# Performance work log

Hardware: AMD Instinct MI355X
Metric: run time of the kernel (lower is better)

The kernel has to match this reference:

```python
import jax, jax.numpy as jnp
import numpy as np

B, L, D, H, HD, K, MLP = 4, 2048, 1024, 16, 64, 24, 4096


def setup_inputs() -> dict:
    key = jax.random.key(0)
    ks = jax.random.split(key, 17)
    f32 = jnp.float32
    rn = lambda k, s, sc=1.0: jax.random.normal(k, s, dtype=f32) * sc
    return {
        'inputs': rn(ks[0], (B, L, D)),
        'eig_vals': jax.random.uniform(ks[1], (K,), dtype=f32),  # positive eigenvalues
        'eig_vecs': rn(ks[2], (L, K), 1.0 / np.sqrt(L)),
        'w_filters': rn(ks[3], (K, D), 1.0 / np.sqrt(K)),        # lecun_normal-ish
        'w_inputs': rn(ks[4], (D, D), 1.0 / np.sqrt(D)),
        'ln1_scale': jnp.ones((D,), f32),
        'ln1_bias': jnp.zeros((D,), f32),
        'wq': rn(ks[5], (D, H, HD), 1.0 / np.sqrt(D)),
        'wk': rn(ks[6], (D, H, HD), 1.0 / np.sqrt(D)),
        'wv': rn(ks[7], (D, H, HD), 1.0 / np.sqrt(D)),
        'wo': rn(ks[8], (H, HD, D), 1.0 / np.sqrt(D)),
        'ln2_scale': jnp.ones((D,), f32),
        'ln2_bias': jnp.zeros((D,), f32),
        'mlp_w1': rn(ks[9], (D, MLP), 1.0 / np.sqrt(D)),
        'mlp_b1': jnp.zeros((MLP,), f32),
        'mlp_w2': rn(ks[10], (MLP, D), 1.0 / np.sqrt(MLP)),
        'mlp_b2': jnp.zeros((D,), f32),
    }


def _layer_norm(x, scale, bias, eps=1e-6):
    m = jnp.mean(x, axis=-1, keepdims=True)
    v = jnp.var(x, axis=-1, keepdims=True)
    return (x - m) * jax.lax.rsqrt(v + eps) * scale + bias


def reference(inputs, eig_vals, eig_vecs, w_filters, w_inputs,
              ln1_scale, ln1_bias, wq, wk, wv, wo,
              ln2_scale, ln2_bias, mlp_w1, mlp_b1, mlp_w2, mlp_b2):
    seq = inputs.shape[1]
    # --- STU spectral long convolution ---
    rescaled = eig_vecs * eig_vals[None, :] ** 0.25            # [L,K]
    filters = jnp.einsum('lk,kd->ld', rescaled, w_filters)      # [L,D]
    xi = jnp.einsum('bli,id->bld', inputs, w_inputs)            # [B,L,D]
    # causal per-channel conv: out[b,l,d] = sum_t filters[t,d]*xi[b,l-t,d]
    # == full convolve truncated to first L; do it as one batched FFT conv.
    n = 2 * seq
    F = jnp.fft.rfft(filters, n=n, axis=0)                      # [n//2+1, D]
    X = jnp.fft.rfft(xi, n=n, axis=1)                           # [B, n//2+1, D]
    projection = jnp.fft.irfft(X * F[None], n=n, axis=1)[:, :seq, :]
    stu_outs = projection                                       # make_stu_residual=False

    # --- self attention (pre-LN) ---
    x = _layer_norm(stu_outs, ln1_scale, ln1_bias)
    hd = wq.shape[-1]
    q = jnp.einsum('bld,dhk->blhk', x, wq) / jnp.sqrt(jnp.asarray(hd, x.dtype))
    k = jnp.einsum('bld,dhk->blhk', x, wk)
    v = jnp.einsum('bld,dhk->blhk', x, wv)
    attn = jax.nn.softmax(jnp.einsum('bqhk,bshk->bhqs', q, k), axis=-1)
    a = jnp.einsum('bhqs,bshk->bqhk', attn, v)
    a = jnp.einsum('bqhk,hkd->bqd', a, wo)
    x = a + stu_outs

    # --- MLP block (pre-LN) ---
    y = _layer_norm(x, ln2_scale, ln2_bias)
    y = jax.nn.gelu(jnp.einsum('bld,df->blf', y, mlp_w1) + mlp_b1)
    y = jnp.einsum('blf,fd->bld', y, mlp_w2) + mlp_b2
    return x + y
```

## Files before the change

kernel.cpp:

```cpp
#include <hip/hip_runtime.h>
#include <math.h>

#define B_ 4
#define L_ 2048
#define D_ 1024
#define H_ 16
#define HD_ 64
#define K_ 24
#define MLP_ 4096

typedef unsigned short u16;
typedef short s16x8 __attribute__((ext_vector_type(8)));
typedef float fx4 __attribute__((ext_vector_type(4)));
typedef _Float16 h2 __attribute__((ext_vector_type(2)));

__device__ __forceinline__ u16 f2bf(float f) {
    unsigned u = __float_as_uint(f);
    unsigned r = (u + 0x7fff + ((u >> 16) & 1)) >> 16;
    return (u16)r;
}

__device__ __forceinline__ u16 f2h(float f) {
    _Float16 hv = (_Float16)f;
    return __builtin_bit_cast(u16, hv);
}

__device__ __forceinline__ float gelu_t(float x) {
    float u = 0.7978845608028654f * (x + 0.044715f * x * x * x);
    return x / (1.f + __expf(-2.f * u));
}

__device__ __forceinline__ void gload_lds16(const void* g, void* l) {
    __builtin_amdgcn_global_load_lds(
        (const __attribute__((address_space(1))) unsigned int*)g,
        (__attribute__((address_space(3))) unsigned int*)l, 16, 0, 0);
}

#define SBAR() do { __builtin_amdgcn_sched_barrier(0); \
                    __builtin_amdgcn_s_barrier(); \
                    __builtin_amdgcn_sched_barrier(0); } while (0)

__global__ __launch_bounds__(256) void filters_T(const float* __restrict__ eig_vals,
                                                 const float* __restrict__ eig_vecs,
                                                 const float* __restrict__ w_filters,
                                                 u16* __restrict__ outT) {
    int l0 = blockIdx.x * 64, d0 = blockIdx.y * 64;
    __shared__ float ev25[K_];
    __shared__ float rr[64][25];
    __shared__ float wfs[K_][64];
    int tid = threadIdx.x;
    if (tid < K_) ev25[tid] = powf(eig_vals[tid], 0.25f);
    __syncthreads();
    for (int i = tid; i < 64 * K_; i += 256)
        rr[i / K_][i % K_] = eig_vecs[l0 * K_ + i];
    for (int i = tid; i < K_ * 64; i += 256) {
        int k = i >> 6, dd = i & 63;
        wfs[k][dd] = ev25[k] * w_filters[k * D_ + d0 + dd];
    }
    __syncthreads();
    int lane = tid & 63, w = tid >> 6;
    float acc[16];
#pragma unroll
    for (int i = 0; i < 16; i++) acc[i] = 0.f;
#pragma unroll
    for (int k = 0; k < K_; k++) {
        float rv = rr[lane][k];
#pragma unroll
        for (int i = 0; i < 16; i++) acc[i] += rv * wfs[k][w * 16 + i];
    }
#pragma unroll
    for (int i = 0; i < 16; i++)
        outT[(size_t)(d0 + w * 16 + i) * L_ + l0 + (lane ^ 63)] = f2h(acc[i]);
}

__global__ __launch_bounds__(256) void cast_bf16(const float* __restrict__ in,
                                                 u16* __restrict__ out) {
    int i = blockIdx.x * 256 + threadIdx.x;
    float4 v = ((const float4*)in)[i];
    ushort4 o;
    o.x = f2bf(v.x); o.y = f2bf(v.y); o.z = f2bf(v.z); o.w = f2bf(v.w);
    ((ushort4*)out)[i] = o;
}

struct CastJobs {
    const float* src[8];
    u16* dst[8];
    int R[8], C[8];
    int off[8];
};

__global__ __launch_bounds__(256) void cast_T_all(CastJobs J) {
    __shared__ float t[32][33];
    int bid = blockIdx.x;
    int j = 0;
#pragma unroll
    for (int k = 1; k < 8; k++)
        if (bid >= J.off[k]) j = k;
    int local = bid - J.off[j];
    int R = J.R[j], C = J.C[j];
    int nbx = C >> 5;
    int lsh = __ffs(nbx) - 1;
    int bx = local & (nbx - 1), by = local >> lsh;
    const float* in = J.src[j];
    u16* out = J.dst[j];
    int c0 = bx * 32, r0 = by * 32;
    int tx = threadIdx.x & 31, ty = threadIdx.x >> 5;
#pragma unroll
    for (int p = 0; p < 4; p++)
        t[ty + p * 8][tx] = in[(size_t)(r0 + ty + p * 8) * C + c0 + tx];
    __syncthreads();
#pragma unroll
    for (int p = 0; p < 4; p++)
        out[(size_t)(c0 + ty + p * 8) * R + r0 + tx] = f2bf(t[tx][ty + p * 8]);
}

__global__ __launch_bounds__(512, 2) void gemm_bf16(
    const u16* __restrict__ A, const u16* __restrict__ Bt,
    float* __restrict__ C, u16* __restrict__ Cb,
    int M, int N, int K, float alpha,
    const float* __restrict__ bias, const float* __restrict__ resid, int act,
    int qcols, int f16out) {
    __shared__ __align__(16) u16 lds[3 * 24576];
    const int SLOT = 24576;
    const int BOFF = 8192;

    int tid = threadIdx.x;
    int wid = tid >> 6, lane = tid & 63;
    int quad = lane >> 4, l15 = lane & 15;
    int rb = wid >> 2, cb = wid & 3;

    int bxs = blockIdx.x, bys = blockIdx.y;
    if ((gridDim.y & 7) == 0) {
        int bid = blockIdx.x + gridDim.x * blockIdx.y;
        int xcd = bid & 7, idx = bid >> 3;
        bys = xcd + 8 * (idx / gridDim.x);
        bxs = idx % gridDim.x;
    }
    int bm = bys * 128, bn = bxs * 256;
    int nt = K >> 6;

    int qoffe = (quad * 8) ^ ((l15 & 4) ? 16 : 0);
    int aRd = (rb * 64 + l15) * 64 + qoffe;
    int bRd = BOFF + (cb * 64 + l15) * 64 + qoffe;

    int srow = wid * 8 + (lane >> 3);
    int scole = ((lane & 7) * 8) ^ ((lane & 32) ? 16 : 0);
    const u16* Ag = A + (size_t)(bm + srow) * K + scole;
    const u16* Bg = Bt + (size_t)(bn + srow) * K + scole;
    int ldst = wid * 512;

#define STAGE_A(s, t, c) gload_lds16(Ag + (size_t)(c) * 64 * K + (size_t)(t) * 64, \
                                     &lds[(s) * SLOT + (c) * 4096 + ldst])
#define STAGE_B(s, t, c) gload_lds16(Bg + (size_t)(c) * 64 * K + (size_t)(t) * 64, \
                                     &lds[(s) * SLOT + BOFF + (c) * 4096 + ldst])

    STAGE_A(0, 0, 0); STAGE_A(0, 0, 1);
    STAGE_B(0, 0, 0); STAGE_B(0, 0, 1); STAGE_B(0, 0, 2); STAGE_B(0, 0, 3);
    STAGE_A(1, 1, 0); STAGE_A(1, 1, 1);
    STAGE_B(1, 1, 0); STAGE_B(1, 1, 1); STAGE_B(1, 1, 2); STAGE_B(1, 1, 3);
    asm volatile("s_waitcnt vmcnt(6)" ::: "memory");
    SBAR();

    fx4 acc[4][4];
#pragma unroll
    for (int i = 0; i < 4; i++)
#pragma unroll
        for (int j = 0; j < 4; j++) acc[i][j] = (fx4){0.f, 0.f, 0.f, 0.f};

    int sa = 0, sb = 1, sc = 2;
    for (int t = 0; t < nt; t++) {
        int ts = (t + 2 < nt) ? t + 2 : nt - 1;
        const u16* ap = &lds[sa * SLOT + aRd];
        const u16* bp = &lds[sa * SLOT + bRd];
        s16x8 a[4], b[2][4];
#pragma unroll
        for (int mf = 0; mf < 4; mf++) a[mf] = *(const s16x8*)(ap + mf * 1024);
#pragma unroll
        for (int kk = 0; kk < 2; kk++)
#pragma unroll
            for (int nf = 0; nf < 4; nf++)
                b[kk][nf] = *(const s16x8*)(bp + nf * 1024 + kk * 32);
        STAGE_A(sc, ts, 0); STAGE_A(sc, ts, 1); STAGE_B(sc, ts, 0);
        SBAR();
        asm volatile("s_waitcnt lgkmcnt(0)" ::: "memory");
        __builtin_amdgcn_sched_barrier(0);
        __builtin_amdgcn_s_setprio(1);
#pragma unroll
        for (int nf = 0; nf < 4; nf++)
#pragma unroll
            for (int mf = 0; mf < 4; mf++)
                acc[mf][nf] = __builtin_amdgcn_mfma_f32_16x16x32_bf16(
                    a[mf], b[0][nf], acc[mf][nf], 0, 0, 0);
        __builtin_amdgcn_s_setprio(0);
        SBAR();
#pragma unroll
        for (int mf = 0; mf < 4; mf++)
            a[mf] = *(const s16x8*)(ap + mf * 1024 + 32);
        STAGE_B(sc, ts, 1); STAGE_B(sc, ts, 2); STAGE_B(sc, ts, 3);
        SBAR();
        asm volatile("s_waitcnt lgkmcnt(0)" ::: "memory");
        __builtin_amdgcn_sched_barrier(0);
        __builtin_amdgcn_s_setprio(1);
#pragma unroll
        for (int nf = 0; nf < 4; nf++)
#pragma unroll
            for (int mf = 0; mf < 4; mf++)
                acc[mf][nf] = __builtin_amdgcn_mfma_f32_16x16x32_bf16(
                    a[mf], b[1][nf], acc[mf][nf], 0, 0, 0);
        __builtin_amdgcn_s_setprio(0);
        asm volatile("s_waitcnt vmcnt(6)" ::: "memory");
        __builtin_amdgcn_sched_barrier(0);
        SBAR();
        int tmp = sa; sa = sb; sb = sc; sc = tmp;
    }
#undef STAGE_A
#undef STAGE_B

    if (f16out) {
        asm volatile("s_waitcnt vmcnt(0)" ::: "memory");
        __syncthreads();
        u16* tb = lds;
#pragma unroll
        for (int mf = 0; mf < 4; mf++)
#pragma unroll
            for (int nf = 0; nf < 4; nf++) {
                int c = cb * 64 + nf * 16 + l15;
                int r = rb * 64 + mf * 16 + quad * 4;
#pragma unroll
                for (int reg = 0; reg < 4; reg++)
                    tb[c * 136 + r + reg] = f2h(acc[mf][nf][reg]);
            }
        __syncthreads();
#pragma unroll
        for (int it = 0; it < 8; it++) {
            int c = (tid >> 4) + it * 32;
            int r0 = (tid & 15) * 8;
            uint4 v4 = *(const uint4*)&tb[c * 136 + r0];
            *(uint4*)&Cb[(size_t)(bn + c) * M + bm + r0] = v4;
        }
        return;
    }

#pragma unroll
    for (int mf = 0; mf < 4; mf++) {
        int row0 = bm + rb * 64 + mf * 16 + quad * 4;
#pragma unroll
        for (int nf = 0; nf < 4; nf++) {
            int col = bn + cb * 64 + nf * 16 + l15;
            float a2 = (col < qcols) ? alpha * 0.125f : alpha;
            float bv = bias ? bias[col] : 0.f;
#pragma unroll
            for (int reg = 0; reg < 4; reg++) {
                float v = a2 * acc[mf][nf][reg] + bv;
                if (act) v = gelu_t(v);
                size_t idx = (size_t)(row0 + reg) * N + col;
                if (resid) v += resid[idx];
                if (C) C[idx] = v;
                else Cb[idx] = f2bf(v);
            }
        }
    }
}

__global__ __launch_bounds__(256, 6) void conv_k(const u16* __restrict__ FT,
                                                 const u16* __restrict__ XT,
                                                 float* __restrict__ OUT) {
    int bid = blockIdx.x + 16 * (blockIdx.y + 16 * blockIdx.z);
    int xcd = bid & 7, ix = bid >> 3;
    int group = xcd * 8 + (ix >> 4);
    int xblk = ix & 15;
    int d0 = (group & 15) * 64, b = group >> 4;

    __shared__ u16 xs[64][132];
    __shared__ u16 ftr[64][68];
    int tid = threadIdx.x;
    int dd = tid & 63;
    int jg = tid >> 6;
    int L0 = jg * 16;
    int frow = tid >> 3, fq = (tid & 7) * 8;
    int xrow = tid >> 4, xq = (tid & 15) * 8;
    const u16* fbase = FT + (size_t)(d0 + frow) * L_ + fq;
    const u16* xbase = XT + (size_t)(d0 + xrow) * (B_ * L_) + (size_t)b * L_ + xq;

#pragma unroll 1
    for (int half = 0; half < 2; half++) {
        int lt = half ? (31 - xblk) : xblk;
        int l0 = lt * 64;
        float acc[16];
#pragma unroll
        for (int i = 0; i < 16; i++) acc[i] = 0.f;

        for (int t0 = 0; t0 <= l0; t0 += 64) {
            int jb = l0 - t0 - 64;
#pragma unroll
            for (int p = 0; p < 2; p++) {
                uint4 Fq = *(const uint4*)(fbase + (size_t)p * 32 * L_ + t0);
                *(uint2*)&ftr[frow + p * 32][fq] = make_uint2(Fq.x, Fq.y);
                *(uint2*)&ftr[frow + p * 32][fq + 4] = make_uint2(Fq.z, Fq.w);
            }
            if (jb >= 0) {
#pragma unroll
                for (int p = 0; p < 4; p++) {
                    uint4 Xq = *(const uint4*)(xbase + (size_t)p * 16 * (B_ * L_) + jb);
                    *(uint2*)&xs[xrow + p * 16][xq] = make_uint2(Xq.x, Xq.y);
                    *(uint2*)&xs[xrow + p * 16][xq + 4] = make_uint2(Xq.z, Xq.w);
                }
            } else {
#pragma unroll
                for (int p = 0; p < 4; p++) {
                    uint4 Xq = make_uint4(0, 0, 0, 0);
                    if (xq >= 64)
                        Xq = *(const uint4*)(xbase + (size_t)p * 16 * (B_ * L_) - 64);
                    *(uint2*)&xs[xrow + p * 16][xq] = make_uint2(Xq.x, Xq.y);
                    *(uint2*)&xs[xrow + p * 16][xq + 4] = make_uint2(Xq.z, Xq.w);
                }
            }
            __syncthreads();

            unsigned Q[10], E[10];
            {
                uint2 q0 = *(const uint2*)&xs[dd][L0];
                uint2 q1 = *(const uint2*)&xs[dd][L0 + 4];
                uint2 q2 = *(const uint2*)&xs[dd][L0 + 8];
                uint2 q3 = *(const uint2*)&xs[dd][L0 + 12];
                Q[0] = q0.x; Q[1] = q0.y; Q[2] = q1.x; Q[3] = q1.y;
                Q[4] = q2.x; Q[5] = q2.y; Q[6] = q3.x; Q[7] = q3.y;
#pragma unroll
                for (int j = 0; j < 7; j++)
                    E[j] = __builtin_amdgcn_alignbit(Q[j + 1], Q[j], 16);
            }
#pragma unroll
            for (int s = 0; s < 16; s++) {
                const int h = (2 * s) % 10;
                uint2 nx = *(const uint2*)&xs[dd][L0 + 16 + 4 * s];
                Q[(h + 8) % 10] = nx.x;
                Q[(h + 9) % 10] = nx.y;
                E[(h + 7) % 10] = __builtin_amdgcn_alignbit(Q[(h + 8) % 10], Q[(h + 7) % 10], 16);
                E[(h + 8) % 10] = __builtin_amdgcn_alignbit(Q[(h + 9) % 10], Q[(h + 8) % 10], 16);
                uint2 fr = *(const uint2*)&ftr[dd][4 * s];
                h2 f01 = __builtin_bit_cast(h2, fr.x);
                h2 f23 = __builtin_bit_cast(h2, fr.y);
#pragma unroll
                for (int i = 0; i < 16; i += 2) {
                    const int p = (h + i / 2) % 10;
                    const int p1 = (h + i / 2 + 1) % 10;
                    const int p2 = (h + i / 2 + 2) % 10;
                    acc[i] = __builtin_amdgcn_fdot2(f01, __builtin_bit_cast(h2, E[p]), acc[i], false);
                    acc[i] = __builtin_amdgcn_fdot2(f23, __builtin_bit_cast(h2, E[p1]), acc[i], false);
                    acc[i + 1] = __builtin_amdgcn_fdot2(f01, __builtin_bit_cast(h2, Q[p1]), acc[i + 1], false);
                    acc[i + 1] = __builtin_amdgcn_fdot2(f23, __builtin_bit_cast(h2, Q[p2]), acc[i + 1], false);
                }
            }
            __syncthreads();
        }
#pragma unroll
        for (int i = 0; i < 16; i++)
            OUT[((size_t)b * L_ + l0 + L0 + i) * D_ + d0 + dd] = acc[i];
    }
}

__global__ __launch_bounds__(256) void layernorm_bf16(const float* __restrict__ x,
                                                      const float* __restrict__ scale,
                                                      const float* __restrict__ bias,
                                                      u16* __restrict__ y) {
    size_t row = blockIdx.x;
    int tid = threadIdx.x;
    const float4 v = *(const float4*)&x[row * D_ + tid * 4];
    float s = v.x + v.y + v.z + v.w;
    float q = v.x * v.x + v.y * v.y + v.z * v.z + v.w * v.w;
#pragma unroll
    for (int off = 32; off >= 1; off >>= 1) {
        s += __shfl_xor(s, off, 64);
        q += __shfl_xor(q, off, 64);
    }
    __shared__ float ss[4], sq[4];
    int w = tid >> 6;
    if ((tid & 63) == 0) { ss[w] = s; sq[w] = q; }
    __syncthreads();
    s = ss[0] + ss[1] + ss[2] + ss[3];
    q = sq[0] + sq[1] + sq[2] + sq[3];
    float mean = s * (1.f / D_);
    float var = q * (1.f / D_) - mean * mean;
    float r = rsqrtf(var + 1e-6f);
    const float4 sc = *(const float4*)&scale[tid * 4];
    const float4 bi = *(const float4*)&bias[tid * 4];
    ushort4 o;
    o.x = f2bf((v.x - mean) * r * sc.x + bi.x);
    o.y = f2bf((v.y - mean) * r * sc.y + bi.y);
    o.z = f2bf((v.z - mean) * r * sc.z + bi.z);
    o.w = f2bf((v.w - mean) * r * sc.w + bi.w);
    *(ushort4*)&y[row * D_ + tid * 4] = o;
}

__global__ __launch_bounds__(256) void attn_mfma(const u16* __restrict__ Qg,
                                                 const u16* __restrict__ Kg,
                                                 const u16* __restrict__ Vg,
                                                 u16* __restrict__ Og) {
    const int QSTR = 3072;
    int bxs = blockIdx.x, bys = blockIdx.y;
    {
        int bid = blockIdx.x + gridDim.x * blockIdx.y;
        int xcd = bid & 7, idx = bid >> 3;
        bys = xcd + 8 * (idx / gridDim.x);
        bxs = idx % gridDim.x;
    }
    int q0 = bxs * 128;
    int b = bys >> 4, h = bys & 15;
    __shared__ __align__(16) u16 qs[128 * 72];
    __shared__ __align__(16) u16 ks[64 * 72];
    __shared__ __align__(16) u16 vt[64 * 72];
    int tid = threadIdx.x;
    int w = tid >> 6, lane = tid & 63;
    int quad = lane >> 4, l15 = lane & 15;
    const size_t base = (size_t)b * L_ * QSTR + h * HD_;

#pragma unroll
    for (int i = tid; i < 128 * 8; i += 256) {
        int r = i >> 3, c = i & 7;
        *(uint4*)&qs[r * 72 + c * 8] =
            *(const uint4*)&Qg[base + (size_t)(q0 + r) * QSTR + c * 8];
    }
    __syncthreads();
    s16x8 aq[2][2];
#pragma unroll
    for (int mi = 0; mi < 2; mi++)
#pragma unroll
        for (int kb = 0; kb < 2; kb++)
            aq[mi][kb] = *(const s16x8*)&qs[(w * 32 + mi * 16 + l15) * 72 + kb * 32 + quad * 8];

    float rsacc[2][4];
    fx4 o[2][4];
#pragma unroll
    for (int mi = 0; mi < 2; mi++)
#pragma unroll
        for (int i = 0; i < 4; i++) {
            rsacc[mi][i] = 0.f;
            o[mi][i] = (fx4){0.f, 0.f, 0.f, 0.f};
        }
    u16* psw = qs + w * 32 * 72;

    int kr0 = tid >> 3, kc = tid & 7;
    const u16* kg0 = Kg + base + (size_t)kr0 * QSTR + kc * 8;
    const u16* kg1 = kg0 + (size_t)32 * QSTR;
    const u16* vg = Vg + base + (size_t)lane * QSTR + w * 8;
    uint4 kp0 = *(const uint4*)kg0;
    uint4 kp1 = *(const uint4*)kg1;
    uint4 vp0 = *(const uint4*)vg;
    uint4 vp1 = *(const uint4*)(vg + 32);

    for (int s0 = 0; s0 < L_; s0 += 64) {
        __syncthreads();
        *(uint4*)&ks[kr0 * 72 + kc * 8] = kp0;
        *(uint4*)&ks[(kr0 + 32) * 72 + kc * 8] = kp1;
        {
            u16 t0[8], t1[8];
            *(uint4*)t0 = vp0;
            *(uint4*)t1 = vp1;
#pragma unroll
            for (int j = 0; j < 8; j++) vt[(w * 8 + j) * 72 + lane] = t0[j];
#pragma unroll
            for (int j = 0; j < 8; j++) vt[(w * 8 + 32 + j) * 72 + lane] = t1[j];
        }
        if (s0 + 64 < L_) {
            size_t off = (size_t)(s0 + 64) * QSTR;
            kp0 = *(const uint4*)(kg0 + off);
            kp1 = *(const uint4*)(kg1 + off);
            vp0 = *(const uint4*)(vg + off);
            vp1 = *(const uint4*)(vg + off + 32);
        }
        __syncthreads();

        fx4 sv[2][4];
#pragma unroll
        for (int mi = 0; mi < 2; mi++)
#pragma unroll
            for (int nt = 0; nt < 4; nt++) sv[mi][nt] = (fx4){0.f, 0.f, 0.f, 0.f};
        __builtin_amdgcn_s_setprio(1);
#pragma unroll
        for (int kb = 0; kb < 2; kb++)
#pragma unroll
            for (int nt = 0; nt < 4; nt++) {
                s16x8 bk = *(const s16x8*)&ks[(nt * 16 + l15) * 72 + kb * 32 + quad * 8];
#pragma unroll
                for (int mi = 0; mi < 2; mi++)
                    sv[mi][nt] = __builtin_amdgcn_mfma_f32_16x16x32_bf16(
                        aq[mi][kb], bk, sv[mi][nt], 0, 0, 0);
            }
        __builtin_amdgcn_s_setprio(0);

#pragma unroll
        for (int mi = 0; mi < 2; mi++)
#pragma unroll
            for (int nt = 0; nt < 4; nt++) {
                float p0 = __expf(sv[mi][nt][0]);
                float p1 = __expf(sv[mi][nt][1]);
                float p2 = __expf(sv[mi][nt][2]);
                float p3 = __expf(sv[mi][nt][3]);
                rsacc[mi][0] += p0; rsacc[mi][1] += p1;
                rsacc[mi][2] += p2; rsacc[mi][3] += p3;
                unsigned pk01, pk23;
                asm("v_cvt_pk_bf16_f32 %0, %1, %2" : "=v"(pk01) : "v"(p0), "v"(p1));
                asm("v_cvt_pk_bf16_f32 %0, %1, %2" : "=v"(pk23) : "v"(p2), "v"(p3));
                int basei = (mi * 16 + quad * 4) * 72 + nt * 16 + l15;
                psw[basei]       = (u16)pk01;
                psw[basei + 72]  = (u16)(pk01 >> 16);
                psw[basei + 144] = (u16)pk23;
                psw[basei + 216] = (u16)(pk23 >> 16);
            }

        __builtin_amdgcn_s_setprio(1);
#pragma unroll
        for (int kb = 0; kb < 2; kb++) {
            s16x8 ap[2];
#pragma unroll
            for (int mi = 0; mi < 2; mi++)
                ap[mi] = *(const s16x8*)&psw[(mi * 16 + l15) * 72 + kb * 32 + quad * 8];
#pragma unroll
            for (int nt = 0; nt < 4; nt++) {
                s16x8 bv = *(const s16x8*)&vt[(nt * 16 + l15) * 72 + kb * 32 + quad * 8];
#pragma unroll
                for (int mi = 0; mi < 2; mi++)
                    o[mi][nt] = __builtin_amdgcn_mfma_f32_16x16x32_bf16(
                        ap[mi], bv, o[mi][nt], 0, 0, 0);
            }
        }
        __builtin_amdgcn_s_setprio(0);
    }
    float lsum[2][4];
#pragma unroll
    for (int mi = 0; mi < 2; mi++)
#pragma unroll
        for (int reg = 0; reg < 4; reg++) {
            float r = rsacc[mi][reg];
#pragma unroll
            for (int off = 8; off >= 1; off >>= 1)
                r += __shfl_xor(r, off, 16);
            lsum[mi][reg] = r;
        }
    const size_t baseo = (size_t)b * L_ * 1024 + h * HD_;
#pragma unroll
    for (int mi = 0; mi < 2; mi++)
#pragma unroll
        for (int reg = 0; reg < 4; reg++) {
            float inv = 1.f / lsum[mi][reg];
            size_t row = baseo +
                (size_t)(q0 + w * 32 + mi * 16 + quad * 4 + reg) * 1024;
#pragma unroll
            for (int nt = 0; nt < 4; nt++)
                Og[row + nt * 16 + l15] = f2bf(o[mi][nt][reg] * inv);
        }
}

extern "C" void kernel_launch(void* const* d_in, const int* in_sizes, int n_in,
                              void* d_out, int out_size, void* d_ws, size_t ws_size,
                              hipStream_t stream) {
    const float* inputs   = (const float*)d_in[0];
    const float* eig_vals = (const float*)d_in[1];
    const float* eig_vecs = (const float*)d_in[2];
    const float* w_filt   = (const float*)d_in[3];
    const float* w_inp    = (const float*)d_in[4];
    const float* ln1_s    = (const float*)d_in[5];
    const float* ln1_b    = (const float*)d_in[6];
    const float* wq       = (const float*)d_in[7];
    const float* wk       = (const float*)d_in[8];
    const float* wv       = (const float*)d_in[9];
    const float* wo       = (const float*)d_in[10];
    const float* ln2_s    = (const float*)d_in[11];
    const float* ln2_b    = (const float*)d_in[12];
    const float* w1       = (const float*)d_in[13];
    const float* b1       = (const float*)d_in[14];
    const float* w2       = (const float*)d_in[15];
    const float* b2       = (const float*)d_in[16];
    float* out = (float*)d_out;
    char* ws = (char*)d_ws;
    const size_t MB = 1u << 20;
    u16*   INb   = (u16*)(ws + 0 * MB);
    u16*   WIt   = (u16*)(ws + 16 * MB);
    u16*   WQKVt = (u16*)(ws + 18 * MB);
    u16*   WOt   = (u16*)(ws + 24 * MB);
    u16*   W1t   = (u16*)(ws + 26 * MB);
    u16*   W2t   = (u16*)(ws + 34 * MB);
    u16*   HID   = (u16*)(ws + 48 * MB);
    u16*   XIT   = (u16*)(ws + 64 * MB);
    float* STU   = (float*)(ws + 80 * MB);
    u16*   XN    = (u16*)(ws + 112 * MB);
    u16*   QKV   = (u16*)(ws + 128 * MB);
    float* Xb    = (float*)(ws + 128 * MB);
    u16*   YN    = (u16*)(ws + 160 * MB);
    u16*   FvT   = (u16*)(ws + 176 * MB);
    u16*   Ab    = (u16*)(ws + 176 * MB);

    const int M = B_ * L_;

    cast_bf16<<<(M * D_ / 4 + 255) / 256, 256, 0, stream>>>(inputs, INb);

    CastJobs J;
    J.src[0] = w_inp; J.dst[0] = WIt;               J.R[0] = D_;   J.C[0] = D_;
    J.src[1] = wq;    J.dst[1] = WQKVt + 0 * D_ * D_; J.R[1] = D_; J.C[1] = D_;
    J.src[2] = wk;    J.dst[2] = WQKVt + 1 * D_ * D_; J.R[2] = D_; J.C[2] = D_;
    J.src[3] = wv;    J.dst[3] = WQKVt + 2 * D_ * D_; J.R[3] = D_; J.C[3] = D_;
    J.src[4] = wo;    J.dst[4] = WOt;               J.R[4] = D_;   J.C[4] = D_;
    J.src[5] = w1;    J.dst[5] = W1t;               J.R[5] = D_;   J.C[5] = MLP_;
    J.src[6] = w2;    J.dst[6] = W2t;               J.R[6] = MLP_; J.C[6] = D_;
    J.src[7] = w_inp; J.dst[7] = WIt;               J.R[7] = D_;   J.C[7] = D_;
    int nb = 0;
    for (int j = 0; j < 7; j++) {
        J.off[j] = nb;
        nb += (J.C[j] / 32) * (J.R[j] / 32);
    }
    J.off[7] = nb;
    cast_T_all<<<nb, 256, 0, stream>>>(J);

    filters_T<<<dim3(L_ / 64, D_ / 64), 256, 0, stream>>>(eig_vals, eig_vecs, w_filt, FvT);

    gemm_bf16<<<dim3(D_ / 256, M / 128), 512, 0, stream>>>(
        INb, WIt, nullptr, XIT, M, D_, D_, 1.f, nullptr, nullptr, 0, 0, 1);
    conv_k<<<dim3(16, D_ / 64, B_), 256, 0, stream>>>(FvT, XIT, STU);
    layernorm_bf16<<<M, 256, 0, stream>>>(STU, ln1_s, ln1_b, XN);
    gemm_bf16<<<dim3(3 * D_ / 256, M / 128), 512, 0, stream>>>(
        XN, WQKVt, nullptr, QKV, M, 3 * D_, D_, 1.f, nullptr, nullptr, 0, D_, 0);
    attn_mfma<<<dim3(L_ / 128, B_ * H_), 256, 0, stream>>>(
        QKV, QKV + D_, QKV + 2 * D_, Ab);
    gemm_bf16<<<dim3(D_ / 256, M / 128), 512, 0, stream>>>(
        Ab, WOt, Xb, nullptr, M, D_, D_, 1.f, nullptr, STU, 0, 0, 0);
    layernorm_bf16<<<M, 256, 0, stream>>>(Xb, ln2_s, ln2_b, YN);
    gemm_bf16<<<dim3(MLP_ / 256, M / 128), 512, 0, stream>>>(
        YN, W1t, nullptr, HID, M, MLP_, D_, 1.f, b1, nullptr, 1, 0, 0);
    gemm_bf16<<<dim3(D_ / 256, M / 128), 512, 0, stream>>>(
        HID, W2t, out, nullptr, M, D_, MLP_, 1.f, b2, Xb, 0, 0, 0);
}
```

Before: 806.1 us.

## Prefetch next conv tiles into registers and drop a GEMM barrier

The causal convolution kernel now loads the next filter and input tile from global memory into registers right after the current tile is written to shared memory, so those loads overlap with the current tile's compute. The GEMM main loop also drops one workgroup barrier between the first MFMA phase and the next A-fragment reads. The prefetch adds register pressure. Removing the barrier could risk a shared-memory race if the following stage writes overlap data still being read.

```diff
diff --git a/kernel.cpp b/kernel.cpp
--- a/kernel.cpp
+++ b/kernel.cpp
@@ -192,7 +192,6 @@
                 acc[mf][nf] = __builtin_amdgcn_mfma_f32_16x16x32_bf16(
                     a[mf], b[0][nf], acc[mf][nf], 0, 0, 0);
         __builtin_amdgcn_s_setprio(0);
-        SBAR();
 #pragma unroll
         for (int mf = 0; mf < 4; mf++)
             a[mf] = *(const s16x8*)(ap + mf * 1024 + 32);
@@ -290,32 +289,60 @@
 #pragma unroll
         for (int i = 0; i < 16; i++) acc[i] = 0.f;
 
+        uint4 Fp[2], Xp[4];
+        {
+            int jb = l0 - 64;
+#pragma unroll
+            for (int p = 0; p < 2; p++)
+                Fp[p] = *(const uint4*)(fbase + (size_t)p * 32 * L_);
+            if (jb >= 0) {
+#pragma unroll
+                for (int p = 0; p < 4; p++)
+                    Xp[p] = *(const uint4*)(xbase + (size_t)p * 16 * (B_ * L_) + jb);
+            } else {
+#pragma unroll
+                for (int p = 0; p < 4; p++) {
+                    uint4 z = make_uint4(0, 0, 0, 0);
+                    if (xq >= 64)
+                        z = *(const uint4*)(xbase + (size_t)p * 16 * (B_ * L_) - 64);
+                    Xp[p] = z;
+                }
+            }
+        }
+
         for (int t0 = 0; t0 <= l0; t0 += 64) {
-            int jb = l0 - t0 - 64;
 #pragma unroll
             for (int p = 0; p < 2; p++) {
-                uint4 Fq = *(const uint4*)(fbase + (size_t)p * 32 * L_ + t0);
-                *(uint2*)&ftr[frow + p * 32][fq] = make_uint2(Fq.x, Fq.y);
-                *(uint2*)&ftr[frow + p * 32][fq + 4] = make_uint2(Fq.z, Fq.w);
-            }
-            if (jb >= 0) {
-#pragma unroll
-                for (int p = 0; p < 4; p++) {
-                    uint4 Xq = *(const uint4*)(xbase + (size_t)p * 16 * (B_ * L_) + jb);
-                    *(uint2*)&xs[xrow + p * 16][xq] = make_uint2(Xq.x, Xq.y);
-                    *(uint2*)&xs[xrow + p * 16][xq + 4] = make_uint2(Xq.z, Xq.w);
+                *(uint2*)&ftr[frow + p * 32][fq] = make_uint2(Fp[p].x, Fp[p].y);
+                *(uint2*)&ftr[frow + p * 32][fq + 4] = make_uint2(Fp[p].z, Fp[p].w);
+            }
+#pragma unroll
+            for (int p = 0; p < 4; p++) {
+                *(uint2*)&xs[xrow + p * 16][xq] = make_uint2(Xp[p].x, Xp[p].y);
+                *(uint2*)&xs[xrow + p * 16][xq + 4] = make_uint2(Xp[p].z, Xp[p].w);
+            }
+            __syncthreads();
+
+            if (t0 + 64 <= l0) {
+                int t1 = t0 + 64;
+                int jb = l0 - t1 - 64;
+#pragma unroll
+                for (int p = 0; p < 2; p++)
+                    Fp[p] = *(const uint4*)(fbase + (size_t)p * 32 * L_ + t1);
+                if (jb >= 0) {
+#pragma unroll
+                    for (int p = 0; p < 4; p++)
+                        Xp[p] = *(const uint4*)(xbase + (size_t)p * 16 * (B_ * L_) + jb);
+                } else {
+#pragma unroll
+                    for (int p = 0; p < 4; p++) {
+                        uint4 z = make_uint4(0, 0, 0, 0);
+                        if (xq >= 64)
+                            z = *(const uint4*)(xbase + (size_t)p * 16 * (B_ * L_) - 64);
+                        Xp[p] = z;
+                    }
                 }
-            } else {
-#pragma unroll
-                for (int p = 0; p < 4; p++) {
-                    uint4 Xq = make_uint4(0, 0, 0, 0);
-                    if (xq >= 64)
-                        Xq = *(const uint4*)(xbase + (size_t)p * 16 * (B_ * L_) - 64);
-                    *(uint2*)&xs[xrow + p * 16][xq] = make_uint2(Xq.x, Xq.y);
-                    *(uint2*)&xs[xrow + p * 16][xq + 4] = make_uint2(Xq.z, Xq.w);
-                }
-            }
-            __syncthreads();
+            }
 
             unsigned Q[10], E[10];
             {
```

Result: slower. 825.4 us (+2.4%).
